# Kernel tuning notes

Hardware: AMD Instinct MI355X
Metric: run time of the kernel (lower is better)

The kernel has to match this reference:

```python
import jax, jax.numpy as jnp
import numpy as np

DIM = 768
NUM_HEADS = 12
HEAD_DIM = DIM // NUM_HEADS
SCALE = HEAD_DIM ** -0.5


def setup_inputs() -> dict:
    key = jax.random.key(0)
    ks = jax.random.split(key, 5)
    b, n = 8, 1024
    x = jax.random.normal(ks[0], (b, n, DIM), dtype=jnp.float32)
    # qkv Linear weight: torch stores (out, in) = (3*DIM, DIM)
    w_qkv = jax.random.normal(ks[1], (3 * DIM, DIM), dtype=jnp.float32) * (DIM ** -0.5)
    q_bias = jax.random.normal(ks[2], (DIM,), dtype=jnp.float32) * 0.02
    v_bias = jax.random.normal(ks[3], (DIM,), dtype=jnp.float32) * 0.02
    w_proj = jax.random.normal(ks[4], (DIM, DIM), dtype=jnp.float32) * (DIM ** -0.5)
    b_proj = jnp.zeros((DIM,), dtype=jnp.float32)
    return {"x": x, "w_qkv": w_qkv, "q_bias": q_bias, "v_bias": v_bias,
            "w_proj": w_proj, "b_proj": b_proj}


def reference(x, w_qkv, q_bias, v_bias, w_proj, b_proj):
    b, n, _ = x.shape
    # qkv bias: [q_bias, zeros, v_bias]
    qkv_bias = jnp.concatenate([q_bias, jnp.zeros_like(v_bias), v_bias])
    qkv = x @ w_qkv.T + qkv_bias                      # (b, n, 3*DIM)
    qkv = qkv.reshape(b, n, 3, NUM_HEADS, HEAD_DIM)
    qkv = jnp.transpose(qkv, (2, 0, 3, 1, 4))          # (3, b, h, n, d)
    q, k, v = qkv[0], qkv[1], qkv[2]
    q = q * SCALE
    attn = jnp.einsum('bhqd,bhkd->bhqk', q, k)         # (b, h, n, n)
    attn = jax.nn.softmax(attn, axis=-1)
    out = jnp.einsum('bhqk,bhkd->bhqd', attn, v)       # (b, h, n, d)
    out = jnp.transpose(out, (0, 2, 1, 3)).reshape(b, n, NUM_HEADS * HEAD_DIM)
    return out @ w_proj.T + b_proj
```

## Files before the change

### kernel.cpp

```cpp
#include <hip/hip_runtime.h>
#include <math.h>

#define BATCH 8
#define SEQ   1024
#define DIM   768
#define NH    12
#define HD    64
#define MROWS 8192
#define NQKV  2304
#define KDIM  768
#define QSCALE 0.18033688011112042f

typedef unsigned short u16;
typedef unsigned int   u32;
typedef __attribute__((ext_vector_type(8))) short bf16x8;
typedef __attribute__((ext_vector_type(4))) float f32x4;
typedef __attribute__((ext_vector_type(16))) float f32x16;

__device__ __forceinline__ u16 f2bf(float f){
  u32 u = __builtin_bit_cast(u32, f);
  u += 0x7FFFu + ((u >> 16) & 1u);
  return (u16)(u >> 16);
}

__device__ __forceinline__ void gload16(const void* g, void* l){
  __builtin_amdgcn_global_load_lds((const __attribute__((address_space(1))) u32*)g,
                                   (__attribute__((address_space(3))) u32*)l, 16, 0, 0);
}

__device__ __forceinline__ f32x16 zero16(){
  return (f32x16){0.f,0.f,0.f,0.f,0.f,0.f,0.f,0.f,0.f,0.f,0.f,0.f,0.f,0.f,0.f,0.f};
}

__global__ __launch_bounds__(256) void convert_bf16(
    const float* __restrict__ x, const float* __restrict__ wq,
    const float* __restrict__ wp, u16* __restrict__ xb,
    u16* __restrict__ wqb, u16* __restrict__ wpb){
  const long n1 = (long)MROWS*DIM/8, n2 = (long)NQKV*DIM/8, n3 = (long)DIM*DIM/8;
  long i = (long)blockIdx.x*blockDim.x + threadIdx.x;
  const float* s; u16* d;
  if (i < n1)            { s = x  + i*8;        d = xb  + i*8; }
  else if (i < n1+n2)    { long j=i-n1;    s = wq + j*8; d = wqb + j*8; }
  else if (i < n1+n2+n3) { long j=i-n1-n2; s = wp + j*8; d = wpb + j*8; }
  else return;
  float4 a = ((const float4*)s)[0];
  float4 b = ((const float4*)s)[1];
  union { u16 h[8]; uint4 v; } o;
  o.h[0]=f2bf(a.x); o.h[1]=f2bf(a.y); o.h[2]=f2bf(a.z); o.h[3]=f2bf(a.w);
  o.h[4]=f2bf(b.x); o.h[5]=f2bf(b.y); o.h[6]=f2bf(b.z); o.h[7]=f2bf(b.w);
  *((uint4*)d) = o.v;
}


__global__ __launch_bounds__(512, 4) void qkv_gemm(
    const u16* __restrict__ xb, const u16* __restrict__ wb,
    const float* __restrict__ qbias, const float* __restrict__ vbias,
    u16* __restrict__ qo, u16* __restrict__ ko, u16* __restrict__ vto){
  __shared__ u16 As[16384];
  __shared__ u16 Bs[16384];
  const int tid = threadIdx.x;
  const int wid = tid >> 6, lane = tid & 63;
  const int lr = lane & 15, lg = lane >> 4;
  const int wm = wid >> 2, wn = wid & 3;
  const int swz = (blockIdx.x & 7) * 144 + (blockIdx.x >> 3);
  const int bm = swz / 18, bn = swz % 18;
  const int mbase = bm * 128, nbase = bn * 128;
  const int sr8 = tid >> 3;
  const int sc8 = ((tid & 7) ^ (sr8 & 7)) * 8;
  const u16* aS = xb + (size_t)(mbase + sr8) * KDIM + sc8;
  const u16* bS = wb + (size_t)(nbase + sr8) * KDIM + sc8;
  u16* aD = As + tid * 8;
  u16* bD = Bs + tid * 8;

#define STAGEQ(buf, k0) do {                                                  \
    gload16(aS + (k0),            aD + (buf)*8192);                           \
    gload16(aS + (k0) + 64*KDIM,  aD + (buf)*8192 + 4096);                    \
    gload16(bS + (k0),            bD + (buf)*8192);                           \
    gload16(bS + (k0) + 64*KDIM,  bD + (buf)*8192 + 4096);                    \
  } while(0)

  f32x4 acc[4][2];
  #pragma unroll
  for (int a=0;a<4;++a)
    #pragma unroll
    for (int b=0;b<2;++b) acc[a][b] = (f32x4){0.f,0.f,0.f,0.f};

  STAGEQ(0, 0);
  __syncthreads();

  for (int kt = 0; kt < 12; ++kt){
    const int cur = kt & 1;
    if (kt < 11) STAGEQ(cur ^ 1, (kt+1)*64);
    const u16* Ac = As + cur*8192;
    const u16* Bc = Bs + cur*8192;
    bf16x8 af[2][4], bfv[2][2];
    #pragma unroll
    for (int kk = 0; kk < 2; ++kk){
      const int ch = (((kk*4 + lg)) ^ (lr & 7)) * 8;
      #pragma unroll
      for (int f = 0; f < 4; ++f)
        af[kk][f]  = *(const bf16x8*)(Ac + (wm*64 + f*16 + lr)*64 + ch);
      #pragma unroll
      for (int g = 0; g < 2; ++g)
        bfv[kk][g] = *(const bf16x8*)(Bc + (wn*32 + g*16 + lr)*64 + ch);
    }
    #pragma unroll
    for (int fm = 0; fm < 4; ++fm)
      #pragma unroll
      for (int fn = 0; fn < 2; ++fn){
        acc[fm][fn] = __builtin_amdgcn_mfma_f32_16x16x32_bf16(af[0][fm], bfv[0][fn], acc[fm][fn], 0,0,0);
        acc[fm][fn] = __builtin_amdgcn_mfma_f32_16x16x32_bf16(af[1][fm], bfv[1][fn], acc[fm][fn], 0,0,0);
      }
    __syncthreads();
  }
#undef STAGEQ

  const int which = bn / 6;
  const int bb = mbase >> 10, nn0 = mbase & 1023;
  if (which == 2){
    const int vcol0 = nbase - 1536;
    float bv[2];
    #pragma unroll
    for (int fn = 0; fn < 2; ++fn) bv[fn] = vbias[vcol0 + wn*32 + fn*16 + lr];
    u16* Ls = As;
    #pragma unroll
    for (int h = 0; h < 2; ++h){
      __syncthreads();
      if (wm == h){
        #pragma unroll
        for (int fn = 0; fn < 2; ++fn){
          const int n = wn*32 + fn*16 + lr;
          #pragma unroll
          for (int fm = 0; fm < 4; ++fm)
            #pragma unroll
            for (int r = 0; r < 4; ++r){
              const int mloc = fm*16 + lg*4 + r;
              Ls[n*64 + (((mloc>>3) ^ (n&7))*8) + (mloc&7)] = f2bf(acc[fm][fn][r] + bv[fn]);
            }
        }
      }
      __syncthreads();
      const int n = tid >> 2, q4 = tid & 3;
      const int col = vcol0 + n;
      u16* drow = vto + ((size_t)((bb*NH + (col>>6))*HD + (col&63)))*SEQ + nn0 + h*64;
      #pragma unroll
      for (int j2 = 0; j2 < 2; ++j2){
        const int j = q4*2 + j2;
        *(uint4*)(drow + j*8) = *(const uint4*)(Ls + n*64 + ((j ^ (n&7))*8));
      }
    }
  } else {
    const int mrow0 = mbase + wm*64;
    const int ncol0 = nbase - which*768 + wn*32;
    #pragma unroll
    for (int fn = 0; fn < 2; ++fn){
      const int col = ncol0 + fn*16 + lr;
      const int hh = col >> 6, dd = col & 63;
      const float bias = (which == 0) ? qbias[col] : 0.f;
      #pragma unroll
      for (int fm = 0; fm < 4; ++fm){
        #pragma unroll
        for (int r = 0; r < 4; ++r){
          const int m = mrow0 + fm*16 + lg*4 + r;
          const int head = (m >> 10)*NH + hh;
          const float v = acc[fm][fn][r] + bias;
          if (which == 0) qo[((size_t)head*SEQ + (m & 1023))*HD + dd] = f2bf(v * QSCALE);
          else            ko[((size_t)head*SEQ + (m & 1023))*HD + dd] = f2bf(v);
        }
      }
    }
  }
}

__global__ __launch_bounds__(256, 3) void attn_kernel(
    const u16* __restrict__ qg, const u16* __restrict__ kg,
    const u16* __restrict__ vtg, u16* __restrict__ og){
  __shared__ u16 Ks[3*4096];
  __shared__ u16 VTs[3*4096];
  const int tid  = threadIdx.x;
  const int wid  = tid >> 6, lane = tid & 63;
  const int l31  = lane & 31, hi = lane >> 5, l7 = lane & 7;
  const int bid  = blockIdx.x;
  const int swz  = (bid & 7) * 96 + (bid >> 3);
  const int head = swz >> 3;
  const int qbase = (swz & 7) * 128;
  const u16* Q  = qg  + (size_t)head * SEQ * HD;
  const u16* K  = kg  + (size_t)head * SEQ * HD;
  const u16* VT = vtg + (size_t)head * HD * SEQ;

  const int qrow = qbase + wid*32 + l31;
  bf16x8 qf[4];
  #pragma unroll
  for (int dc = 0; dc < 4; ++dc)
    qf[dc] = *(const bf16x8*)(Q + (size_t)qrow*HD + dc*16 + hi*8);

  f32x16 oacc[2];
  oacc[0] = zero16(); oacc[1] = zero16();
  float lrow = 0.f;

  const int srow   = lane >> 3;
  const int schunk = ((lane & 7) ^ srow) * 8;

#define STAGE(bufi, kv0) do {                                                 \
    const u16* ksrc = K + (size_t)((kv0) + wid*16 + srow)*HD + schunk;        \
    gload16(ksrc,         &Ks[(bufi)*4096 + wid*1024]);                       \
    gload16(ksrc + 8*HD,  &Ks[(bufi)*4096 + wid*1024 + 512]);                 \
    const u16* vsrc = VT + (size_t)(wid*16 + srow)*SEQ + (kv0) + schunk;      \
    gload16(vsrc,         &VTs[(bufi)*4096 + wid*1024]);                      \
    gload16(vsrc + 8*SEQ, &VTs[(bufi)*4096 + wid*1024 + 512]);                \
  } while(0)

  STAGE(0, 0);
  STAGE(1, 64);

  #pragma unroll
  for (int t = 0; t < 16; ++t){
    const int cur = t % 3;
    if (t < 15) asm volatile("s_waitcnt vmcnt(4)" ::: "memory");
    else        asm volatile("s_waitcnt vmcnt(0)" ::: "memory");
    __builtin_amdgcn_s_barrier();
    if (t < 14) STAGE((t+2)%3, (t+2)*64);

    const u16* Kc  = &Ks[cur*4096];
    const u16* VTc = &VTs[cur*4096];

    f32x16 sv[2];
    __builtin_amdgcn_s_setprio(1);
    #pragma unroll
    for (int b = 0; b < 2; ++b){
      sv[b] = zero16();
      #pragma unroll
      for (int dc = 0; dc < 4; ++dc){
        bf16x8 kf = *(const bf16x8*)(&Kc[(b*32 + l31)*64 + (((dc*2 + hi) ^ l7) * 8)]);
        sv[b] = __builtin_amdgcn_mfma_f32_32x32x16_bf16(kf, qf[dc], sv[b], 0,0,0);
      }
    }
    __builtin_amdgcn_s_setprio(0);

    float tsum[16];
    #pragma unroll
    for (int i = 0; i < 16; ++i){
      float p0 = __builtin_amdgcn_exp2f(sv[0][i]);
      float p1 = __builtin_amdgcn_exp2f(sv[1][i]);
      sv[0][i] = p0; sv[1][i] = p1;
      tsum[i] = p0 + p1;
    }
    #pragma unroll
    for (int st = 8; st > 0; st >>= 1)
      #pragma unroll
      for (int i = 0; i < st; ++i) tsum[i] += tsum[i + st];
    const float ssum = tsum[0];
    lrow += ssum + __shfl_xor(ssum, 32);

    bf16x8 pa[4];
    #pragma unroll
    for (int b = 0; b < 2; ++b){
      u32 x0,x1,x2,x3,y0,y1,y2,y3;
      asm("v_cvt_pk_bf16_f32 %0, %1, %2" : "=v"(x0) : "v"(sv[b][0]),  "v"(sv[b][1]));
      asm("v_cvt_pk_bf16_f32 %0, %1, %2" : "=v"(y0) : "v"(sv[b][4]),  "v"(sv[b][5]));
      asm("v_cvt_pk_bf16_f32 %0, %1, %2" : "=v"(x1) : "v"(sv[b][2]),  "v"(sv[b][3]));
      asm("v_cvt_pk_bf16_f32 %0, %1, %2" : "=v"(y1) : "v"(sv[b][6]),  "v"(sv[b][7]));
      asm("v_permlane32_swap_b32 %0, %1" : "+v"(x0), "+v"(y0));
      asm("v_permlane32_swap_b32 %0, %1" : "+v"(x1), "+v"(y1));
      asm("v_cvt_pk_bf16_f32 %0, %1, %2" : "=v"(x2) : "v"(sv[b][8]),  "v"(sv[b][9]));
      asm("v_cvt_pk_bf16_f32 %0, %1, %2" : "=v"(y2) : "v"(sv[b][12]), "v"(sv[b][13]));
      asm("v_cvt_pk_bf16_f32 %0, %1, %2" : "=v"(x3) : "v"(sv[b][10]), "v"(sv[b][11]));
      asm("v_cvt_pk_bf16_f32 %0, %1, %2" : "=v"(y3) : "v"(sv[b][14]), "v"(sv[b][15]));
      asm("v_permlane32_swap_b32 %0, %1" : "+v"(x2), "+v"(y2));
      asm("v_permlane32_swap_b32 %0, %1" : "+v"(x3), "+v"(y3));
      union { u32 w[4]; bf16x8 f; } fa, fb;
      fa.w[0]=x0; fa.w[1]=x1; fa.w[2]=y0; fa.w[3]=y1;
      fb.w[0]=x2; fb.w[1]=x3; fb.w[2]=y2; fb.w[3]=y3;
      pa[b*2]   = fa.f;
      pa[b*2+1] = fb.f;
    }

    __builtin_amdgcn_s_setprio(1);
    #pragma unroll
    for (int kc = 0; kc < 4; ++kc){
      #pragma unroll
      for (int db = 0; db < 2; ++db){
        bf16x8 vf = *(const bf16x8*)(&VTc[(db*32 + l31)*64 + (((kc*2 + hi) ^ l7) * 8)]);
        oacc[db] = __builtin_amdgcn_mfma_f32_32x32x16_bf16(pa[kc], vf, oacc[db], 0,0,0);
      }
    }
    __builtin_amdgcn_s_setprio(0);
  }
#undef STAGE

  const float inv = 1.f / lrow;
  const int bb = head / NH, hh = head % NH;
  #pragma unroll
  for (int r = 0; r < 16; ++r){
    const int q = (r&3) + 8*(r>>2) + 4*hi;
    const float s = __shfl(inv, q);
    const int n = qbase + wid*32 + q;
    u16* orow = og + (size_t)(bb*SEQ + n)*DIM + hh*HD;
    orow[l31]      = f2bf(oacc[0][r] * s);
    orow[32 + l31] = f2bf(oacc[1][r] * s);
  }
}

__global__ __launch_bounds__(512, 4) void proj_gemm(
    const u16* __restrict__ ab, const u16* __restrict__ wb,
    const float* __restrict__ bias, float* __restrict__ out){
  __shared__ u16 As[16384];
  __shared__ u16 Bs[16384];
  const int tid = threadIdx.x;
  const int wid = tid >> 6, lane = tid & 63;
  const int lr = lane & 15, lg = lane >> 4;
  const int wm = wid >> 2, wn = wid & 3;
  const int swz = (blockIdx.x & 7) * 48 + (blockIdx.x >> 3);
  const int bm = swz / 6, bn = swz % 6;
  const int mbase = bm * 128, nbase = bn * 128;
  const int sr8 = tid >> 3;
  const int sc8 = ((tid & 7) ^ (sr8 & 7)) * 8;
  const u16* aS = ab + (size_t)(mbase + sr8) * KDIM + sc8;
  const u16* bS = wb + (size_t)(nbase + sr8) * KDIM + sc8;
  u16* aD = As + tid * 8;
  u16* bD = Bs + tid * 8;

#define STAGEP(buf, k0) do {                                                  \
    gload16(aS + (k0),            aD + (buf)*8192);                           \
    gload16(aS + (k0) + 64*KDIM,  aD + (buf)*8192 + 4096);                    \
    gload16(bS + (k0),            bD + (buf)*8192);                           \
    gload16(bS + (k0) + 64*KDIM,  bD + (buf)*8192 + 4096);                    \
  } while(0)

  f32x4 acc[4][2];
  #pragma unroll
  for (int a=0;a<4;++a)
    #pragma unroll
    for (int b=0;b<2;++b) acc[a][b] = (f32x4){0.f,0.f,0.f,0.f};

  STAGEP(0, 0);
  __syncthreads();

  for (int kt = 0; kt < 12; ++kt){
    const int cur = kt & 1;
    if (kt < 11) STAGEP(cur ^ 1, (kt+1)*64);
    const u16* Ac = As + cur*8192;
    const u16* Bc = Bs + cur*8192;
    bf16x8 af[2][4], bfv[2][2];
    #pragma unroll
    for (int kk = 0; kk < 2; ++kk){
      const int ch = (((kk*4 + lg)) ^ (lr & 7)) * 8;
      #pragma unroll
      for (int f = 0; f < 4; ++f)
        af[kk][f]  = *(const bf16x8*)(Ac + (wm*64 + f*16 + lr)*64 + ch);
      #pragma unroll
      for (int g = 0; g < 2; ++g)
        bfv[kk][g] = *(const bf16x8*)(Bc + (wn*32 + g*16 + lr)*64 + ch);
    }
    #pragma unroll
    for (int fm = 0; fm < 4; ++fm)
      #pragma unroll
      for (int fn = 0; fn < 2; ++fn){
        acc[fm][fn] = __builtin_amdgcn_mfma_f32_16x16x32_bf16(af[0][fm], bfv[0][fn], acc[fm][fn], 0,0,0);
        acc[fm][fn] = __builtin_amdgcn_mfma_f32_16x16x32_bf16(af[1][fm], bfv[1][fn], acc[fm][fn], 0,0,0);
      }
    __syncthreads();
  }
#undef STAGEP

  const int mrow0 = mbase + wm*64;
  const int ncol0 = nbase + wn*32;
  #pragma unroll
  for (int fn = 0; fn < 2; ++fn){
    const int col = ncol0 + fn*16 + lr;
    const float bv = bias[col];
    #pragma unroll
    for (int fm = 0; fm < 4; ++fm){
      #pragma unroll
      for (int r = 0; r < 4; ++r){
        const int m = mrow0 + fm*16 + lg*4 + r;
        out[(size_t)m*DIM + col] = acc[fm][fn][r] + bv;
      }
    }
  }
}

extern "C" void kernel_launch(void* const* d_in, const int* in_sizes, int n_in,
                              void* d_out, int out_size, void* d_ws, size_t ws_size,
                              hipStream_t stream) {
  const float* x      = (const float*)d_in[0];
  const float* w_qkv  = (const float*)d_in[1];
  const float* q_bias = (const float*)d_in[2];
  const float* v_bias = (const float*)d_in[3];
  const float* w_proj = (const float*)d_in[4];
  const float* b_proj = (const float*)d_in[5];
  float* out = (float*)d_out;
  char* ws = (char*)d_ws;
  u16* xb  = (u16*)(ws);
  u16* wqb = (u16*)(ws + 12582912);
  u16* wpb = (u16*)(ws + 16121856);
  u16* qbf = (u16*)(ws + 17301504);
  u16* kbf = (u16*)(ws + 29884416);
  u16* vtb = (u16*)(ws + 42467328);
  u16* abf = (u16*)(ws + 55050240);

  convert_bf16<<<4224, 256, 0, stream>>>(x, w_qkv, w_proj, xb, wqb, wpb);
  qkv_gemm   <<<64*18, 512, 0, stream>>>(xb, wqb, q_bias, v_bias, qbf, kbf, vtb);
  attn_kernel<<<96*8,  256, 0, stream>>>(qbf, kbf, vtb, abf);
  proj_gemm  <<<64*6,  512, 0, stream>>>(abf, wpb, b_proj, out);
}
```

Baseline: 105.0 us.

## Software-pipeline PV MFMAs across attention iterations and retile projection GEMM

In the attention kernel, the P·V MFMAs for the previous KV tile are deferred into the next iteration and issued right after the QK MFMAs, with V fragments preloaded into registers, so matrix work overlaps the exp/convert phase. The final tile's PV is done after the loop, and the barrier wait now also drains LDS counters. The projection GEMM moves to 64x128 tiles with 256 threads and twice as many blocks, which improves load balance across CUs for this small GEMM. In exchange, the attention kernel holds more live registers, which may lower occupancy.

```diff
diff --git a/kernel.cpp b/kernel.cpp
--- a/kernel.cpp
+++ b/kernel.cpp
@@ -50,7 +50,6 @@
   o.h[4]=f2bf(b.x); o.h[5]=f2bf(b.y); o.h[6]=f2bf(b.z); o.h[7]=f2bf(b.w);
   *((uint4*)d) = o.v;
 }
-
 
 __global__ __launch_bounds__(512, 4) void qkv_gemm(
     const u16* __restrict__ xb, const u16* __restrict__ wb,
@@ -198,6 +197,9 @@
   oacc[0] = zero16(); oacc[1] = zero16();
   float lrow = 0.f;
 
+  bf16x8 vfr[8];
+  bf16x8 pa[4];
+
   const int srow   = lane >> 3;
   const int schunk = ((lane & 7) ^ srow) * 8;
 
@@ -216,8 +218,8 @@
   #pragma unroll
   for (int t = 0; t < 16; ++t){
     const int cur = t % 3;
-    if (t < 15) asm volatile("s_waitcnt vmcnt(4)" ::: "memory");
-    else        asm volatile("s_waitcnt vmcnt(0)" ::: "memory");
+    if (t < 15) asm volatile("s_waitcnt vmcnt(4) lgkmcnt(0)" ::: "memory");
+    else        asm volatile("s_waitcnt vmcnt(0) lgkmcnt(0)" ::: "memory");
     __builtin_amdgcn_s_barrier();
     if (t < 14) STAGE((t+2)%3, (t+2)*64);
 
@@ -235,7 +237,20 @@
         sv[b] = __builtin_amdgcn_mfma_f32_32x32x16_bf16(kf, qf[dc], sv[b], 0,0,0);
       }
     }
+    if (t > 0){
+      #pragma unroll
+      for (int kc = 0; kc < 4; ++kc)
+        #pragma unroll
+        for (int db = 0; db < 2; ++db)
+          oacc[db] = __builtin_amdgcn_mfma_f32_32x32x16_bf16(pa[kc], vfr[kc*2+db], oacc[db], 0,0,0);
+    }
     __builtin_amdgcn_s_setprio(0);
+
+    #pragma unroll
+    for (int kc = 0; kc < 4; ++kc)
+      #pragma unroll
+      for (int db = 0; db < 2; ++db)
+        vfr[kc*2+db] = *(const bf16x8*)(&VTc[(db*32 + l31)*64 + (((kc*2 + hi) ^ l7) * 8)]);
 
     float tsum[16];
     #pragma unroll
@@ -252,7 +267,6 @@
     const float ssum = tsum[0];
     lrow += ssum + __shfl_xor(ssum, 32);
 
-    bf16x8 pa[4];
     #pragma unroll
     for (int b = 0; b < 2; ++b){
       u32 x0,x1,x2,x3,y0,y1,y2,y3;
@@ -274,19 +288,16 @@
       pa[b*2]   = fa.f;
       pa[b*2+1] = fb.f;
     }
-
-    __builtin_amdgcn_s_setprio(1);
-    #pragma unroll
-    for (int kc = 0; kc < 4; ++kc){
-      #pragma unroll
-      for (int db = 0; db < 2; ++db){
-        bf16x8 vf = *(const bf16x8*)(&VTc[(db*32 + l31)*64 + (((kc*2 + hi) ^ l7) * 8)]);
-        oacc[db] = __builtin_amdgcn_mfma_f32_32x32x16_bf16(pa[kc], vf, oacc[db], 0,0,0);
-      }
-    }
-    __builtin_amdgcn_s_setprio(0);
   }
 #undef STAGE
+
+  __builtin_amdgcn_s_setprio(1);
+  #pragma unroll
+  for (int kc = 0; kc < 4; ++kc)
+    #pragma unroll
+    for (int db = 0; db < 2; ++db)
+      oacc[db] = __builtin_amdgcn_mfma_f32_32x32x16_bf16(pa[kc], vfr[kc*2+db], oacc[db], 0,0,0);
+  __builtin_amdgcn_s_setprio(0);
 
   const float inv = 1.f / lrow;
   const int bb = head / NH, hh = head % NH;
@@ -301,37 +312,38 @@
   }
 }
 
-__global__ __launch_bounds__(512, 4) void proj_gemm(
+__global__ __launch_bounds__(256) void proj_gemm(
     const u16* __restrict__ ab, const u16* __restrict__ wb,
     const float* __restrict__ bias, float* __restrict__ out){
-  __shared__ u16 As[16384];
-  __shared__ u16 Bs[16384];
+  __shared__ u16 As2[2*4096];
+  __shared__ u16 Bs2[2*8192];
   const int tid = threadIdx.x;
   const int wid = tid >> 6, lane = tid & 63;
   const int lr = lane & 15, lg = lane >> 4;
-  const int wm = wid >> 2, wn = wid & 3;
-  const int swz = (blockIdx.x & 7) * 48 + (blockIdx.x >> 3);
+  const int wm = wid >> 1, wn = wid & 1;
+  const int swz = (blockIdx.x & 7) * 96 + (blockIdx.x >> 3);
   const int bm = swz / 6, bn = swz % 6;
-  const int mbase = bm * 128, nbase = bn * 128;
+  const int mbase = bm * 64, nbase = bn * 128;
   const int sr8 = tid >> 3;
   const int sc8 = ((tid & 7) ^ (sr8 & 7)) * 8;
   const u16* aS = ab + (size_t)(mbase + sr8) * KDIM + sc8;
   const u16* bS = wb + (size_t)(nbase + sr8) * KDIM + sc8;
-  u16* aD = As + tid * 8;
-  u16* bD = Bs + tid * 8;
+  u16* aD = As2 + tid * 8;
+  u16* bD = Bs2 + tid * 8;
 
 #define STAGEP(buf, k0) do {                                                  \
-    gload16(aS + (k0),            aD + (buf)*8192);                           \
-    gload16(aS + (k0) + 64*KDIM,  aD + (buf)*8192 + 4096);                    \
-    gload16(bS + (k0),            bD + (buf)*8192);                           \
-    gload16(bS + (k0) + 64*KDIM,  bD + (buf)*8192 + 4096);                    \
+    gload16(aS + (k0),            aD + (buf)*4096);                           \
+    gload16(aS + (k0) + 32*KDIM,  aD + (buf)*4096 + 2048);                    \
+    _Pragma("unroll")                                                         \
+    for (int i = 0; i < 4; ++i)                                               \
+      gload16(bS + (k0) + (size_t)i*32*KDIM, bD + (buf)*8192 + i*2048);       \
   } while(0)
 
-  f32x4 acc[4][2];
-  #pragma unroll
-  for (int a=0;a<4;++a)
-    #pragma unroll
-    for (int b=0;b<2;++b) acc[a][b] = (f32x4){0.f,0.f,0.f,0.f};
+  f32x4 acc[2][4];
+  #pragma unroll
+  for (int a=0;a<2;++a)
+    #pragma unroll
+    for (int b=0;b<4;++b) acc[a][b] = (f32x4){0.f,0.f,0.f,0.f};
 
   STAGEP(0, 0);
   __syncthreads();
@@ -339,23 +351,23 @@
   for (int kt = 0; kt < 12; ++kt){
     const int cur = kt & 1;
     if (kt < 11) STAGEP(cur ^ 1, (kt+1)*64);
-    const u16* Ac = As + cur*8192;
-    const u16* Bc = Bs + cur*8192;
-    bf16x8 af[2][4], bfv[2][2];
+    const u16* Ac = As2 + cur*4096;
+    const u16* Bc = Bs2 + cur*8192;
+    bf16x8 af[2][2], bfv[2][4];
     #pragma unroll
     for (int kk = 0; kk < 2; ++kk){
       const int ch = (((kk*4 + lg)) ^ (lr & 7)) * 8;
       #pragma unroll
-      for (int f = 0; f < 4; ++f)
-        af[kk][f]  = *(const bf16x8*)(Ac + (wm*64 + f*16 + lr)*64 + ch);
-      #pragma unroll
-      for (int g = 0; g < 2; ++g)
-        bfv[kk][g] = *(const bf16x8*)(Bc + (wn*32 + g*16 + lr)*64 + ch);
-    }
-    #pragma unroll
-    for (int fm = 0; fm < 4; ++fm)
-      #pragma unroll
-      for (int fn = 0; fn < 2; ++fn){
+      for (int f = 0; f < 2; ++f)
+        af[kk][f]  = *(const bf16x8*)(Ac + (wm*32 + f*16 + lr)*64 + ch);
+      #pragma unroll
+      for (int g = 0; g < 4; ++g)
+        bfv[kk][g] = *(const bf16x8*)(Bc + (wn*64 + g*16 + lr)*64 + ch);
+    }
+    #pragma unroll
+    for (int fm = 0; fm < 2; ++fm)
+      #pragma unroll
+      for (int fn = 0; fn < 4; ++fn){
         acc[fm][fn] = __builtin_amdgcn_mfma_f32_16x16x32_bf16(af[0][fm], bfv[0][fn], acc[fm][fn], 0,0,0);
         acc[fm][fn] = __builtin_amdgcn_mfma_f32_16x16x32_bf16(af[1][fm], bfv[1][fn], acc[fm][fn], 0,0,0);
       }
@@ -363,14 +375,14 @@
   }
 #undef STAGEP
 
-  const int mrow0 = mbase + wm*64;
-  const int ncol0 = nbase + wn*32;
-  #pragma unroll
-  for (int fn = 0; fn < 2; ++fn){
+  const int mrow0 = mbase + wm*32;
+  const int ncol0 = nbase + wn*64;
+  #pragma unroll
+  for (int fn = 0; fn < 4; ++fn){
     const int col = ncol0 + fn*16 + lr;
     const float bv = bias[col];
     #pragma unroll
-    for (int fm = 0; fm < 4; ++fm){
+    for (int fm = 0; fm < 2; ++fm){
       #pragma unroll
       for (int r = 0; r < 4; ++r){
         const int m = mrow0 + fm*16 + lg*4 + r;
@@ -402,5 +414,5 @@
   convert_bf16<<<4224, 256, 0, stream>>>(x, w_qkv, w_proj, xb, wqb, wpb);
   qkv_gemm   <<<64*18, 512, 0, stream>>>(xb, wqb, q_bias, v_bias, qbf, kbf, vtb);
   attn_kernel<<<96*8,  256, 0, stream>>>(qbf, kbf, vtb, abf);
-  proj_gemm  <<<64*6,  512, 0, stream>>>(abf, wpb, b_proj, out);
-}
+  proj_gemm  <<<128*6, 256, 0, stream>>>(abf, wpb, b_proj, out);
+}
```

Result: no change. 106.6 us (+1.5%).
